# Kernel optimization log

Measured on AMD Instinct MI355X. Metric: run time of the kernel, lower is better.

Reference implementation:

```python
import jax, jax.numpy as jnp
import numpy as np

N = 50000
E = 600000
F_IN = 256
H = 128            # num_hidden_units * num_heads (heads=1)
C = 20             # num_classes
NEG_SLOPE = 0.2    # PyG GATConv default


def setup_inputs() -> dict:
    key = jax.random.key(0)
    ks = jax.random.split(key, 16)
    g = lambda k, shape, fan: jax.random.normal(k, shape, jnp.float32) / np.sqrt(fan)
    return {
        "x": jax.random.normal(ks[0], (N, F_IN), jnp.float32),
        "edge_index": jax.random.randint(ks[1], (2, E), 0, N, jnp.int64),
        # GATConv 1: F_IN -> H (heads=1, concat)
        "W1": g(ks[2], (F_IN, H), F_IN),
        "a_src1": g(ks[3], (H,), H),
        "a_dst1": g(ks[4], (H,), H),
        "b1": jnp.zeros((H,), jnp.float32),
        # GATConv 2: H -> H (heads=1)
        "W2": g(ks[5], (H, H), H),
        "a_src2": g(ks[6], (H,), H),
        "a_dst2": g(ks[7], (H,), H),
        "b2": jnp.zeros((H,), jnp.float32),
        # MLP head
        "Wm1": g(ks[8], (H, H), H),
        "bm1": jnp.zeros((H,), jnp.float32),
        "Wm2": g(ks[9], (H, C), H),
        "bm2": jnp.zeros((C,), jnp.float32),
    }


def gat_layer(x, W, a_src, a_dst, b, src, dst, n_nodes):
    """Single-head GATConv (PyG semantics, self-loops already in src/dst)."""
    h = x @ W                                    # [N, H]
    # edge attention logits: leaky_relu(a_src . h_j + a_dst . h_i)
    logits = jax.nn.leaky_relu((h @ a_src)[src] + (h @ a_dst)[dst], NEG_SLOPE)  # [Etot]
    # softmax over incoming edges per target node
    m = jax.ops.segment_max(logits, dst, num_segments=n_nodes)
    e = jnp.exp(logits - m[dst])
    denom = jax.ops.segment_sum(e, dst, num_segments=n_nodes)
    coef = e / denom[dst]                        # [Etot]
    out = jax.ops.segment_sum(coef[:, None] * h[src], dst, num_segments=n_nodes)
    return out + b


def reference(x, edge_index, W1, a_src1, a_dst1, b1, W2, a_src2, a_dst2, b2, Wm1, bm1, Wm2, bm2):
    n = x.shape[0]
    loops = jnp.arange(n, dtype=edge_index.dtype)
    src = jnp.concatenate([edge_index[0], loops])  # add self loops (GATConv default)
    dst = jnp.concatenate([edge_index[1], loops])
    h = gat_layer(x, W1, a_src1, a_dst1, b1, src, dst, n)
    h = jax.nn.relu(h)                            # dropout = identity at eval
    h = gat_layer(h, W2, a_src2, a_dst2, b2, src, dst, n)
    # MLP head: Linear -> (dropout) -> ReLU -> Linear -> sigmoid
    z = jax.nn.relu(h @ Wm1 + bm1)
    return jax.nn.sigmoid(z @ Wm2 + bm2)
```

## Files before the change

### kernel.cpp

```cpp
#include <hip/hip_runtime.h>
#include <math.h>

#define F_IN 256
#define HDIM 128
#define NCLS 20
#define NEG_SLOPE 0.2f
#define SCAN_CHUNK 1024

typedef float f32x4 __attribute__((ext_vector_type(4)));
typedef _Float16 f16x2 __attribute__((ext_vector_type(2)));
typedef _Float16 f16x4 __attribute__((ext_vector_type(4)));
typedef _Float16 f16x8 __attribute__((ext_vector_type(8)));

static __device__ __forceinline__ float lrelu(float x) { return x > 0.f ? x : NEG_SLOPE * x; }

__global__ void count_kernel(const int* __restrict__ ei, int E, int N, int* __restrict__ deg) {
    int e = blockIdx.x * blockDim.x + threadIdx.x;
    int Etot = E + N;
    if (e >= Etot) return;
    int d = (e < E) ? ei[E + e] : (e - E);
    atomicAdd(&deg[d], 1);
}

__global__ __launch_bounds__(256) void scan_reduce_kernel(const int* __restrict__ deg, int n,
                                                          int* __restrict__ bsums) {
    int base = blockIdx.x * SCAN_CHUNK + threadIdx.x * 4;
    int s = 0;
    if (base + 3 < n) {
        int4 v = *reinterpret_cast<const int4*>(&deg[base]);
        s = v.x + v.y + v.z + v.w;
    } else {
#pragma unroll
        for (int j = 0; j < 4; ++j) if (base + j < n) s += deg[base + j];
    }
#pragma unroll
    for (int o = 32; o > 0; o >>= 1) s += __shfl_down(s, o);
    __shared__ int ws[4];
    int lane = threadIdx.x & 63, w = threadIdx.x >> 6;
    if (lane == 0) ws[w] = s;
    __syncthreads();
    if (threadIdx.x == 0) bsums[blockIdx.x] = ws[0] + ws[1] + ws[2] + ws[3];
}

__global__ __launch_bounds__(256) void scan_bsums_kernel(int* __restrict__ bsums, int nb,
                                                         int* __restrict__ off, int n) {
    __shared__ int sh[256];
    int tid = threadIdx.x;
    int v = (tid < nb) ? bsums[tid] : 0;
    sh[tid] = v;
    __syncthreads();
    for (int d = 1; d < 256; d <<= 1) {
        int t = (tid >= d) ? sh[tid - d] : 0;
        __syncthreads();
        sh[tid] += t;
        __syncthreads();
    }
    if (tid < nb) bsums[tid] = sh[tid] - v;
    if (tid == 255) off[n] = sh[255];
}

__global__ __launch_bounds__(256) void scan_down_kernel(const int* __restrict__ deg, int n,
                                                        const int* __restrict__ bpre,
                                                        int* __restrict__ off) {
    int base = blockIdx.x * SCAN_CHUNK + threadIdx.x * 4;
    int v0 = 0, v1 = 0, v2 = 0, v3 = 0;
    if (base + 3 < n) {
        int4 t = *reinterpret_cast<const int4*>(&deg[base]);
        v0 = t.x; v1 = t.y; v2 = t.z; v3 = t.w;
    } else {
        if (base + 0 < n) v0 = deg[base + 0];
        if (base + 1 < n) v1 = deg[base + 1];
        if (base + 2 < n) v2 = deg[base + 2];
        if (base + 3 < n) v3 = deg[base + 3];
    }
    int tsum = v0 + v1 + v2 + v3;
    int lane = threadIdx.x & 63, w = threadIdx.x >> 6;
    int inc = tsum;
#pragma unroll
    for (int o = 1; o < 64; o <<= 1) {
        int t = __shfl_up(inc, o);
        if (lane >= o) inc += t;
    }
    int texc = inc - tsum;
    __shared__ int wsum[4];
    if (lane == 63) wsum[w] = inc;
    __syncthreads();
    int wpre = 0;
    for (int i = 0; i < w; ++i) wpre += wsum[i];
    int p = bpre[blockIdx.x] + wpre + texc;
    if (base + 3 < n) {
        int4 o4;
        o4.x = p; o4.y = p + v0; o4.z = p + v0 + v1; o4.w = p + v0 + v1 + v2;
        *reinterpret_cast<int4*>(&off[base]) = o4;
    } else {
        int run = p;
        if (base + 0 < n) { off[base + 0] = run; run += v0; }
        if (base + 1 < n) { off[base + 1] = run; run += v1; }
        if (base + 2 < n) { off[base + 2] = run; run += v2; }
        if (base + 3 < n) { off[base + 3] = run; }
    }
}

__global__ void scatter_kernel(const int* __restrict__ ei, int E, int N,
                               const int* __restrict__ off, int* __restrict__ cursor,
                               int* __restrict__ csr_src) {
    int e = blockIdx.x * blockDim.x + threadIdx.x;
    int Etot = E + N;
    if (e >= Etot) return;
    int s, d;
    if (e < E) { s = ei[e]; d = ei[E + e]; } else { s = d = e - E; }
    int pos = off[d] + atomicAdd(&cursor[d], 1);
    csr_src[pos] = s;
}

__global__ __launch_bounds__(64) void pack_b_kernel(const float* __restrict__ W1,
                                                    const float* __restrict__ W2,
                                                    const float* __restrict__ Wm1,
                                                    _Float16* __restrict__ p1,
                                                    _Float16* __restrict__ p2,
                                                    _Float16* __restrict__ p3) {
    int t = blockIdx.x;
    int lane = threadIdx.x;
    const float* B; _Float16* out; int r;
    if (t < 64)      { B = W1;  out = p1; r = t; }
    else if (t < 96) { B = W2;  out = p2; r = t - 64; }
    else             { B = Wm1; out = p3; r = t - 96; }
    int ks = r >> 3, cf = r & 7;
    int c  = cf * 16 + (lane & 15);
    int k0 = ks * 32 + (lane >> 4) * 8;
    _Float16 h8[8], l8[8];
#pragma unroll
    for (int i = 0; i < 8; ++i) {
        float v = B[(size_t)(k0 + i) * 128 + c];
        h8[i] = (_Float16)v;
        l8[i] = (_Float16)(v - (float)h8[i]);
    }
    size_t base = (((size_t)(ks * 8 + cf) * 2) * 64 + lane) * 8;
#pragma unroll
    for (int i = 0; i < 8; ++i) { out[base + i] = h8[i]; out[base + 512 + i] = l8[i]; }
}

template <int AFMT>
__global__ __launch_bounds__(256) void gemm_mfma_kernel(const void* __restrict__ Aptr,
                                                        const _Float16* __restrict__ Bp,
                                                        _Float16* __restrict__ C, int M, int K,
                                                        const float* __restrict__ bias, int act) {
    int tid = threadIdx.x;
    int lane = tid & 63;
    int wid = tid >> 6;
    int wr = wid >> 1, wc = wid & 1;
    int bm = blockIdx.x * 64;
    int l15 = lane & 15, l4 = lane >> 4;
    int row0 = bm + wr * 32 + l15;
    int koff = l4 * 8;

    f32x4 acc[2][4];
#pragma unroll
    for (int m = 0; m < 2; ++m)
#pragma unroll
        for (int j = 0; j < 4; ++j) acc[m][j] = (f32x4){0.f, 0.f, 0.f, 0.f};

    const f16x8 zf = {0, 0, 0, 0, 0, 0, 0, 0};

    auto loadA = [&](int ks, f16x8 a[2]) {
        int kbase = ks * 32 + koff;
#pragma unroll
        for (int m = 0; m < 2; ++m) {
            int rr = row0 + m * 16;
            if (rr < M) {
                if (AFMT == 0) {
                    const float* A = (const float*)Aptr;
                    float4 v0 = *reinterpret_cast<const float4*>(&A[(size_t)rr * K + kbase]);
                    float4 v1 = *reinterpret_cast<const float4*>(&A[(size_t)rr * K + kbase + 4]);
                    f16x8 t;
                    t[0] = (_Float16)v0.x; t[1] = (_Float16)v0.y;
                    t[2] = (_Float16)v0.z; t[3] = (_Float16)v0.w;
                    t[4] = (_Float16)v1.x; t[5] = (_Float16)v1.y;
                    t[6] = (_Float16)v1.z; t[7] = (_Float16)v1.w;
                    a[m] = t;
                } else {
                    const _Float16* A = (const _Float16*)Aptr;
                    a[m] = *reinterpret_cast<const f16x8*>(&A[(size_t)rr * K + kbase]);
                }
            } else a[m] = zf;
        }
    };
    auto loadB = [&](int ks, f16x8 bh[4], f16x8 bl[4]) {
#pragma unroll
        for (int j = 0; j < 4; ++j) {
            int cf = wc * 4 + j;
            const _Float16* bp = Bp + (((size_t)(ks * 8 + cf) * 2) * 64 + lane) * 8;
            bh[j] = *reinterpret_cast<const f16x8*>(bp);
            bl[j] = *reinterpret_cast<const f16x8*>(bp + 512);
        }
    };

    f16x8 a0[2], a1[2], bh0[4], bh1[4], bl0[4], bl1[4];
    int ksteps = K >> 5;
    loadA(0, a0); loadB(0, bh0, bl0);
    for (int ks = 0; ks < ksteps; ks += 2) {
        loadA(ks + 1, a1); loadB(ks + 1, bh1, bl1);
#pragma unroll
        for (int j = 0; j < 4; ++j) {
            acc[0][j] = __builtin_amdgcn_mfma_f32_16x16x32_f16(a0[0], bh0[j], acc[0][j], 0, 0, 0);
            acc[1][j] = __builtin_amdgcn_mfma_f32_16x16x32_f16(a0[1], bh0[j], acc[1][j], 0, 0, 0);
            acc[0][j] = __builtin_amdgcn_mfma_f32_16x16x32_f16(a0[0], bl0[j], acc[0][j], 0, 0, 0);
            acc[1][j] = __builtin_amdgcn_mfma_f32_16x16x32_f16(a0[1], bl0[j], acc[1][j], 0, 0, 0);
        }
        if (ks + 2 < ksteps) { loadA(ks + 2, a0); loadB(ks + 2, bh0, bl0); }
#pragma unroll
        for (int j = 0; j < 4; ++j) {
            acc[0][j] = __builtin_amdgcn_mfma_f32_16x16x32_f16(a1[0], bh1[j], acc[0][j], 0, 0, 0);
            acc[1][j] = __builtin_amdgcn_mfma_f32_16x16x32_f16(a1[1], bh1[j], acc[1][j], 0, 0, 0);
            acc[0][j] = __builtin_amdgcn_mfma_f32_16x16x32_f16(a1[0], bl1[j], acc[0][j], 0, 0, 0);
            acc[1][j] = __builtin_amdgcn_mfma_f32_16x16x32_f16(a1[1], bl1[j], acc[1][j], 0, 0, 0);
        }
    }

#pragma unroll
    for (int j = 0; j < 4; ++j) {
        int col = wc * 64 + j * 16 + l15;
        float bi = bias ? bias[col] : 0.f;
#pragma unroll
        for (int m = 0; m < 2; ++m) {
            int rbase = bm + wr * 32 + m * 16 + l4 * 4;
#pragma unroll
            for (int reg = 0; reg < 4; ++reg) {
                int rr = rbase + reg;
                if (rr < M) {
                    float v = acc[m][j][reg] + bi;
                    if (act) v = fmaxf(v, 0.f);
                    C[(size_t)rr * 128 + col] = (_Float16)v;
                }
            }
        }
    }
}

__global__ void alphas_kernel(const _Float16* __restrict__ h, const float* __restrict__ a_src,
                              const float* __restrict__ a_dst, float* __restrict__ as_out,
                              float* __restrict__ ad_out, int N) {
    int wave = (blockIdx.x * blockDim.x + threadIdx.x) >> 6;
    int lane = threadIdx.x & 63;
    if (wave >= N) return;
    f16x2 v  = *reinterpret_cast<const f16x2*>(&h[(size_t)wave * HDIM + 2 * lane]);
    float vx = (float)v[0], vy = (float)v[1];
    float2 as = *reinterpret_cast<const float2*>(&a_src[2 * lane]);
    float2 ad = *reinterpret_cast<const float2*>(&a_dst[2 * lane]);
    float s = vx * as.x + vy * as.y;
    float d = vx * ad.x + vy * ad.y;
#pragma unroll
    for (int o = 32; o > 0; o >>= 1) { s += __shfl_down(s, o); d += __shfl_down(d, o); }
    if (lane == 0) { as_out[wave] = s; ad_out[wave] = d; }
}

__global__ __launch_bounds__(256) void aggregate_kernel(const _Float16* __restrict__ h,
                                 const float* __restrict__ asrc, const float* __restrict__ adst,
                                 const int* __restrict__ off, const int* __restrict__ csr_src,
                                 const float* __restrict__ bias,
                                 _Float16* __restrict__ out,
                                 int N, int do_relu) {
    __shared__ float2 sm[4][64];
    int wslot = threadIdx.x >> 6;
    int wave = blockIdx.x * 4 + wslot;
    int lane = threadIdx.x & 63;
    if (wave >= N) return;
    int n = wave;
    int o0 = off[n], o1 = off[n + 1];
    float ad = adst[n];

    float denom = 0.f;
    float2 accA = make_float2(0.f, 0.f);
    float2 accB = make_float2(0.f, 0.f);

    for (int base = o0; base < o1; base += 64) {
        int cnt = o1 - base; if (cnt > 64) cnt = 64;
        float e = 0.f; int s = 0;
        if (lane < cnt) {
            s = csr_src[base + lane];
            e = __expf(lrelu(asrc[s] + ad));
        }
        float t = e;
#pragma unroll
        for (int o = 32; o > 0; o >>= 1) t += __shfl_xor(t, o);
        denom += t;
        sm[wslot][lane] = make_float2(__int_as_float(s), e);
        int j = 0;
        for (; j + 1 < cnt; j += 2) {
            float2 v0 = sm[wslot][j];
            float2 v1 = sm[wslot][j + 1];
            int s0 = __float_as_int(v0.x);
            int s1 = __float_as_int(v1.x);
            f16x2 h0 = *reinterpret_cast<const f16x2*>(&h[(size_t)s0 * HDIM + 2 * lane]);
            f16x2 h1 = *reinterpret_cast<const f16x2*>(&h[(size_t)s1 * HDIM + 2 * lane]);
            accA.x = fmaf(v0.y, (float)h0[0], accA.x);
            accA.y = fmaf(v0.y, (float)h0[1], accA.y);
            accB.x = fmaf(v1.y, (float)h1[0], accB.x);
            accB.y = fmaf(v1.y, (float)h1[1], accB.y);
        }
        if (j < cnt) {
            float2 v0 = sm[wslot][j];
            int s0 = __float_as_int(v0.x);
            f16x2 h0 = *reinterpret_cast<const f16x2*>(&h[(size_t)s0 * HDIM + 2 * lane]);
            accA.x = fmaf(v0.y, (float)h0[0], accA.x);
            accA.y = fmaf(v0.y, (float)h0[1], accA.y);
        }
    }

    float inv = 1.f / denom;
    float2 bi = *reinterpret_cast<const float2*>(&bias[2 * lane]);
    float r0 = (accA.x + accB.x) * inv + bi.x;
    float r1 = (accA.y + accB.y) * inv + bi.y;
    if (do_relu) { r0 = fmaxf(r0, 0.f); r1 = fmaxf(r1, 0.f); }
    f16x2 o;
    o[0] = (_Float16)r0;
    o[1] = (_Float16)r1;
    *reinterpret_cast<f16x2*>(&out[(size_t)n * HDIM + 2 * lane]) = o;
}

__global__ __launch_bounds__(256) void head_kernel(const _Float16* __restrict__ Z,
                                                   const float* __restrict__ W,
                                                   const float* __restrict__ b,
                                                   float* __restrict__ out, int N) {
    __shared__ float Ws[HDIM][NCLS];
    __shared__ float Zs[256][33];
    int tid = threadIdx.x;
    for (int i = tid; i < HDIM * NCLS; i += 256) Ws[i / NCLS][i % NCLS] = W[i];
    float acc[NCLS];
#pragma unroll
    for (int c = 0; c < NCLS; ++c) acc[c] = 0.f;
    int row = blockIdx.x * 256 + tid;
    for (int k0 = 0; k0 < HDIM; k0 += 32) {
        __syncthreads();
#pragma unroll
        for (int t = 0; t < 8; ++t) {
            int flat = tid * 4 + t * 1024;
            int r = flat >> 5, kk = flat & 31;
            int gr = blockIdx.x * 256 + r;
            if (gr < N) {
                f16x4 v = *reinterpret_cast<const f16x4*>(&Z[(size_t)gr * HDIM + k0 + kk]);
                Zs[r][kk] = (float)v[0]; Zs[r][kk + 1] = (float)v[1];
                Zs[r][kk + 2] = (float)v[2]; Zs[r][kk + 3] = (float)v[3];
            } else {
                Zs[r][kk] = 0.f; Zs[r][kk + 1] = 0.f; Zs[r][kk + 2] = 0.f; Zs[r][kk + 3] = 0.f;
            }
        }
        __syncthreads();
#pragma unroll
        for (int kk = 0; kk < 32; ++kk) {
            float a = Zs[tid][kk];
#pragma unroll
            for (int c = 0; c < NCLS; ++c) acc[c] = fmaf(a, Ws[k0 + kk][c], acc[c]);
        }
    }
    if (row < N) {
#pragma unroll
        for (int c = 0; c < NCLS; ++c) {
            float v = acc[c] + b[c];
            out[(size_t)row * NCLS + c] = 1.f / (1.f + expf(-v));
        }
    }
}

extern "C" void kernel_launch(void* const* d_in, const int* in_sizes, int n_in,
                              void* d_out, int out_size, void* d_ws, size_t ws_size,
                              hipStream_t stream) {
    const float* x      = (const float*)d_in[0];
    const int*   ei     = (const int*)d_in[1];
    const float* W1     = (const float*)d_in[2];
    const float* a_src1 = (const float*)d_in[3];
    const float* a_dst1 = (const float*)d_in[4];
    const float* b1     = (const float*)d_in[5];
    const float* W2     = (const float*)d_in[6];
    const float* a_src2 = (const float*)d_in[7];
    const float* a_dst2 = (const float*)d_in[8];
    const float* b2     = (const float*)d_in[9];
    const float* Wm1    = (const float*)d_in[10];
    const float* bm1    = (const float*)d_in[11];
    const float* Wm2    = (const float*)d_in[12];
    const float* bm2    = (const float*)d_in[13];

    int N = in_sizes[0] / F_IN;
    int E = in_sizes[1] / 2;
    int Etot = E + N;

    char* ws = (char*)d_ws;
    size_t pos = 0;
    auto alloc = [&](size_t bytes) -> void* {
        void* p = ws + pos;
        pos = (pos + bytes + 255) & ~(size_t)255;
        return p;
    };
    _Float16* h16 = (_Float16*)alloc((size_t)N * HDIM * 2);
    _Float16* f16 = (_Float16*)alloc((size_t)N * HDIM * 2);
    float* as_buf = (float*)alloc((size_t)N * 4);
    float* ad_buf = (float*)alloc((size_t)N * 4);
    int*   deg    = (int*)alloc((size_t)N * 4);
    int*   offs   = (int*)alloc((size_t)(N + 1) * 4);
    int*   cursor = (int*)alloc((size_t)N * 4);
    int*   csr    = (int*)alloc((size_t)Etot * 4);
    int*   bsums  = (int*)alloc(256 * 4);
    _Float16* p1 = (_Float16*)alloc(65536 * 2);
    _Float16* p2 = (_Float16*)alloc(32768 * 2);
    _Float16* p3 = (_Float16*)alloc(32768 * 2);

    hipMemsetAsync(deg, 0, (size_t)N * 4, stream);
    hipMemsetAsync(cursor, 0, (size_t)N * 4, stream);

    int eb = (Etot + 255) / 256;
    int nb = (N + SCAN_CHUNK - 1) / SCAN_CHUNK;
    count_kernel<<<eb, 256, 0, stream>>>(ei, E, N, deg);
    scan_reduce_kernel<<<nb, 256, 0, stream>>>(deg, N, bsums);
    scan_bsums_kernel<<<1, 256, 0, stream>>>(bsums, nb, offs, N);
    scan_down_kernel<<<nb, 256, 0, stream>>>(deg, N, bsums, offs);
    scatter_kernel<<<eb, 256, 0, stream>>>(ei, E, N, offs, cursor, csr);

    pack_b_kernel<<<128, 64, 0, stream>>>(W1, W2, Wm1, p1, p2, p3);

    int gemm_blocks = (N + 63) / 64;
    int wave_blocks = (N + 3) / 4;

    gemm_mfma_kernel<0><<<gemm_blocks, 256, 0, stream>>>(x, p1, h16, N, F_IN, nullptr, 0);
    alphas_kernel<<<wave_blocks, 256, 0, stream>>>(h16, a_src1, a_dst1, as_buf, ad_buf, N);
    aggregate_kernel<<<wave_blocks, 256, 0, stream>>>(h16, as_buf, ad_buf, offs, csr, b1, f16, N, 1);

    gemm_mfma_kernel<1><<<gemm_blocks, 256, 0, stream>>>(f16, p2, h16, N, HDIM, nullptr, 0);
    alphas_kernel<<<wave_blocks, 256, 0, stream>>>(h16, a_src2, a_dst2, as_buf, ad_buf, N);
    aggregate_kernel<<<wave_blocks, 256, 0, stream>>>(h16, as_buf, ad_buf, offs, csr, b2, f16, N, 0);

    gemm_mfma_kernel<1><<<gemm_blocks, 256, 0, stream>>>(f16, p3, h16, N, HDIM, bm1, 1);
    head_kernel<<<(N + 255) / 256, 256, 0, stream>>>(h16, Wm2, bm2, (float*)d_out, N);
}
```

Measured before the change: 254.9 us.

## Fuse attention-logit dot products into GEMM epilogue and retile GEMM/aggregation

Removes the separate alphas kernel by computing the a_src/a_dst dot products inside the GEMM epilogue, using shuffles and a small shared-memory reduction across the four waves. The GEMM is retiled to 32-row blocks with each wave owning 32 columns, K is a compile-time template parameter, and loads are prefetched several steps ahead with an interleaved hi/lo B packing. The aggregation kernel now has each half-wave handle alternate edges with 4-wide fp16 loads, and the halves are combined by a cross-half shuffle. This saves a pass over h and two launches, at the cost of more GEMM blocks, more redundant A-row reads, and extra epilogue work. The alphas are now computed from fp32 accumulators rather than fp16-rounded h.

```diff
diff --git a/kernel.cpp b/kernel.cpp
--- a/kernel.cpp
+++ b/kernel.cpp
@@ -128,130 +128,170 @@
     int ks = r >> 3, cf = r & 7;
     int c  = cf * 16 + (lane & 15);
     int k0 = ks * 32 + (lane >> 4) * 8;
-    _Float16 h8[8], l8[8];
+    size_t base = ((size_t)r * 64 + lane) * 16;
 #pragma unroll
     for (int i = 0; i < 8; ++i) {
         float v = B[(size_t)(k0 + i) * 128 + c];
-        h8[i] = (_Float16)v;
-        l8[i] = (_Float16)(v - (float)h8[i]);
-    }
-    size_t base = (((size_t)(ks * 8 + cf) * 2) * 64 + lane) * 8;
-#pragma unroll
-    for (int i = 0; i < 8; ++i) { out[base + i] = h8[i]; out[base + 512 + i] = l8[i]; }
-}
-
-template <int AFMT>
-__global__ __launch_bounds__(256) void gemm_mfma_kernel(const void* __restrict__ Aptr,
-                                                        const _Float16* __restrict__ Bp,
-                                                        _Float16* __restrict__ C, int M, int K,
-                                                        const float* __restrict__ bias, int act) {
+        _Float16 h = (_Float16)v;
+        out[base + i]     = h;
+        out[base + 8 + i] = (_Float16)(v - (float)h);
+    }
+}
+
+template <int AFMT, int KSTEPS>
+__global__ __launch_bounds__(256, 4) void gemm_mfma_kernel(
+        const void* __restrict__ Aptr, const _Float16* __restrict__ Bp,
+        _Float16* __restrict__ C, int M,
+        const float* __restrict__ bias, int act,
+        const float* __restrict__ a_src, const float* __restrict__ a_dst,
+        float* __restrict__ as_out, float* __restrict__ ad_out) {
+    constexpr int K  = KSTEPS * 32;
+    constexpr int DA = (KSTEPS < 3) ? KSTEPS : 3;
+    constexpr int DB = (KSTEPS < 2) ? KSTEPS : 2;
+    __shared__ float sal[2][4][32];
+
     int tid = threadIdx.x;
     int lane = tid & 63;
-    int wid = tid >> 6;
-    int wr = wid >> 1, wc = wid & 1;
-    int bm = blockIdx.x * 64;
+    int wc = tid >> 6;
     int l15 = lane & 15, l4 = lane >> 4;
-    int row0 = bm + wr * 32 + l15;
+    int bm = blockIdx.x * 32;
     int koff = l4 * 8;
 
-    f32x4 acc[2][4];
+    const float*    A32 = (const float*)Aptr;
+    const _Float16* A16 = (const _Float16*)Aptr;
+    int r0 = bm + l15, r1 = bm + l15 + 16;
+    bool ok0 = r0 < M, ok1 = r1 < M;
+    const f16x8 zf = {0, 0, 0, 0, 0, 0, 0, 0};
+    const float4 zf4 = make_float4(0.f, 0.f, 0.f, 0.f);
+
+    float4 sAf[DA][2][2];
+    f16x8  sAh[DA][2];
+    f16x8  sBh[DB][2], sBl[DB][2];
+
+    f32x4 acc[2][2];
 #pragma unroll
     for (int m = 0; m < 2; ++m)
 #pragma unroll
-        for (int j = 0; j < 4; ++j) acc[m][j] = (f32x4){0.f, 0.f, 0.f, 0.f};
-
-    const f16x8 zf = {0, 0, 0, 0, 0, 0, 0, 0};
-
-    auto loadA = [&](int ks, f16x8 a[2]) {
-        int kbase = ks * 32 + koff;
+        for (int j = 0; j < 2; ++j) acc[m][j] = (f32x4){0.f, 0.f, 0.f, 0.f};
+
+    auto issueA = [&](int s) {
+        int slot = s % DA;
+        int kb = s * 32 + koff;
 #pragma unroll
         for (int m = 0; m < 2; ++m) {
-            int rr = row0 + m * 16;
+            int rr = m ? r1 : r0;
+            bool ok = m ? ok1 : ok0;
+            if (AFMT == 0) {
+                const float* p = &A32[(size_t)rr * K + kb];
+                sAf[slot][m][0] = ok ? *reinterpret_cast<const float4*>(p)     : zf4;
+                sAf[slot][m][1] = ok ? *reinterpret_cast<const float4*>(p + 4) : zf4;
+            } else {
+                sAh[slot][m] = ok ? *reinterpret_cast<const f16x8*>(&A16[(size_t)rr * K + kb]) : zf;
+            }
+        }
+    };
+    auto issueB = [&](int s) {
+        int slot = s % DB;
+#pragma unroll
+        for (int j = 0; j < 2; ++j) {
+            int cf = wc * 2 + j;
+            const _Float16* p = Bp + (((size_t)s * 8 + cf) * 64 + lane) * 16;
+            sBh[slot][j] = *reinterpret_cast<const f16x8*>(p);
+            sBl[slot][j] = *reinterpret_cast<const f16x8*>(p + 8);
+        }
+    };
+
+#pragma unroll
+    for (int p = 0; p < DA; ++p) issueA(p);
+#pragma unroll
+    for (int p = 0; p < DB; ++p) issueB(p);
+
+#pragma unroll
+    for (int s = 0; s < KSTEPS; ++s) {
+        f16x8 a[2], bh[2], bl[2];
+        if (AFMT == 0) {
+#pragma unroll
+            for (int m = 0; m < 2; ++m) {
+                float4 u = sAf[s % DA][m][0], w = sAf[s % DA][m][1];
+                f16x8 t;
+                t[0] = (_Float16)u.x; t[1] = (_Float16)u.y;
+                t[2] = (_Float16)u.z; t[3] = (_Float16)u.w;
+                t[4] = (_Float16)w.x; t[5] = (_Float16)w.y;
+                t[6] = (_Float16)w.z; t[7] = (_Float16)w.w;
+                a[m] = t;
+            }
+        } else {
+            a[0] = sAh[s % DA][0];
+            a[1] = sAh[s % DA][1];
+        }
+#pragma unroll
+        for (int j = 0; j < 2; ++j) { bh[j] = sBh[s % DB][j]; bl[j] = sBl[s % DB][j]; }
+        if (s + DA < KSTEPS) issueA(s + DA);
+        if (s + DB < KSTEPS) issueB(s + DB);
+#pragma unroll
+        for (int j = 0; j < 2; ++j) {
+            acc[0][j] = __builtin_amdgcn_mfma_f32_16x16x32_f16(a[0], bh[j], acc[0][j], 0, 0, 0);
+            acc[1][j] = __builtin_amdgcn_mfma_f32_16x16x32_f16(a[1], bh[j], acc[1][j], 0, 0, 0);
+            acc[0][j] = __builtin_amdgcn_mfma_f32_16x16x32_f16(a[0], bl[j], acc[0][j], 0, 0, 0);
+            acc[1][j] = __builtin_amdgcn_mfma_f32_16x16x32_f16(a[1], bl[j], acc[1][j], 0, 0, 0);
+        }
+    }
+
+    float ps[2][4], pd[2][4];
+#pragma unroll
+    for (int m = 0; m < 2; ++m)
+#pragma unroll
+        for (int reg = 0; reg < 4; ++reg) { ps[m][reg] = 0.f; pd[m][reg] = 0.f; }
+
+#pragma unroll
+    for (int j = 0; j < 2; ++j) {
+        int col = wc * 32 + j * 16 + l15;
+        float bi = bias ? bias[col] : 0.f;
+        float asc = a_src ? a_src[col] : 0.f;
+        float adc = a_src ? a_dst[col] : 0.f;
+#pragma unroll
+        for (int m = 0; m < 2; ++m) {
+#pragma unroll
+            for (int reg = 0; reg < 4; ++reg) {
+                int rr = bm + m * 16 + l4 * 4 + reg;
+                float v = acc[m][j][reg] + bi;
+                if (act) v = fmaxf(v, 0.f);
+                if (rr < M) C[(size_t)rr * 128 + col] = (_Float16)v;
+                ps[m][reg] = fmaf(v, asc, ps[m][reg]);
+                pd[m][reg] = fmaf(v, adc, pd[m][reg]);
+            }
+        }
+    }
+
+    if (a_src) {
+#pragma unroll
+        for (int o = 1; o < 16; o <<= 1) {
+#pragma unroll
+            for (int m = 0; m < 2; ++m)
+#pragma unroll
+                for (int reg = 0; reg < 4; ++reg) {
+                    ps[m][reg] += __shfl_xor(ps[m][reg], o);
+                    pd[m][reg] += __shfl_xor(pd[m][reg], o);
+                }
+        }
+        if (l15 == 0) {
+#pragma unroll
+            for (int m = 0; m < 2; ++m)
+#pragma unroll
+                for (int reg = 0; reg < 4; ++reg) {
+                    sal[0][wc][m * 16 + l4 * 4 + reg] = ps[m][reg];
+                    sal[1][wc][m * 16 + l4 * 4 + reg] = pd[m][reg];
+                }
+        }
+        __syncthreads();
+        if (tid < 32) {
+            int rr = bm + tid;
             if (rr < M) {
-                if (AFMT == 0) {
-                    const float* A = (const float*)Aptr;
-                    float4 v0 = *reinterpret_cast<const float4*>(&A[(size_t)rr * K + kbase]);
-                    float4 v1 = *reinterpret_cast<const float4*>(&A[(size_t)rr * K + kbase + 4]);
-                    f16x8 t;
-                    t[0] = (_Float16)v0.x; t[1] = (_Float16)v0.y;
-                    t[2] = (_Float16)v0.z; t[3] = (_Float16)v0.w;
-                    t[4] = (_Float16)v1.x; t[5] = (_Float16)v1.y;
-                    t[6] = (_Float16)v1.z; t[7] = (_Float16)v1.w;
-                    a[m] = t;
-                } else {
-                    const _Float16* A = (const _Float16*)Aptr;
-                    a[m] = *reinterpret_cast<const f16x8*>(&A[(size_t)rr * K + kbase]);
-                }
-            } else a[m] = zf;
-        }
-    };
-    auto loadB = [&](int ks, f16x8 bh[4], f16x8 bl[4]) {
-#pragma unroll
-        for (int j = 0; j < 4; ++j) {
-            int cf = wc * 4 + j;
-            const _Float16* bp = Bp + (((size_t)(ks * 8 + cf) * 2) * 64 + lane) * 8;
-            bh[j] = *reinterpret_cast<const f16x8*>(bp);
-            bl[j] = *reinterpret_cast<const f16x8*>(bp + 512);
-        }
-    };
-
-    f16x8 a0[2], a1[2], bh0[4], bh1[4], bl0[4], bl1[4];
-    int ksteps = K >> 5;
-    loadA(0, a0); loadB(0, bh0, bl0);
-    for (int ks = 0; ks < ksteps; ks += 2) {
-        loadA(ks + 1, a1); loadB(ks + 1, bh1, bl1);
-#pragma unroll
-        for (int j = 0; j < 4; ++j) {
-            acc[0][j] = __builtin_amdgcn_mfma_f32_16x16x32_f16(a0[0], bh0[j], acc[0][j], 0, 0, 0);
-            acc[1][j] = __builtin_amdgcn_mfma_f32_16x16x32_f16(a0[1], bh0[j], acc[1][j], 0, 0, 0);
-            acc[0][j] = __builtin_amdgcn_mfma_f32_16x16x32_f16(a0[0], bl0[j], acc[0][j], 0, 0, 0);
-            acc[1][j] = __builtin_amdgcn_mfma_f32_16x16x32_f16(a0[1], bl0[j], acc[1][j], 0, 0, 0);
-        }
-        if (ks + 2 < ksteps) { loadA(ks + 2, a0); loadB(ks + 2, bh0, bl0); }
-#pragma unroll
-        for (int j = 0; j < 4; ++j) {
-            acc[0][j] = __builtin_amdgcn_mfma_f32_16x16x32_f16(a1[0], bh1[j], acc[0][j], 0, 0, 0);
-            acc[1][j] = __builtin_amdgcn_mfma_f32_16x16x32_f16(a1[1], bh1[j], acc[1][j], 0, 0, 0);
-            acc[0][j] = __builtin_amdgcn_mfma_f32_16x16x32_f16(a1[0], bl1[j], acc[0][j], 0, 0, 0);
-            acc[1][j] = __builtin_amdgcn_mfma_f32_16x16x32_f16(a1[1], bl1[j], acc[1][j], 0, 0, 0);
-        }
-    }
-
-#pragma unroll
-    for (int j = 0; j < 4; ++j) {
-        int col = wc * 64 + j * 16 + l15;
-        float bi = bias ? bias[col] : 0.f;
-#pragma unroll
-        for (int m = 0; m < 2; ++m) {
-            int rbase = bm + wr * 32 + m * 16 + l4 * 4;
-#pragma unroll
-            for (int reg = 0; reg < 4; ++reg) {
-                int rr = rbase + reg;
-                if (rr < M) {
-                    float v = acc[m][j][reg] + bi;
-                    if (act) v = fmaxf(v, 0.f);
-                    C[(size_t)rr * 128 + col] = (_Float16)v;
-                }
+                as_out[rr] = sal[0][0][tid] + sal[0][1][tid] + sal[0][2][tid] + sal[0][3][tid];
+                ad_out[rr] = sal[1][0][tid] + sal[1][1][tid] + sal[1][2][tid] + sal[1][3][tid];
             }
         }
     }
-}
-
-__global__ void alphas_kernel(const _Float16* __restrict__ h, const float* __restrict__ a_src,
-                              const float* __restrict__ a_dst, float* __restrict__ as_out,
-                              float* __restrict__ ad_out, int N) {
-    int wave = (blockIdx.x * blockDim.x + threadIdx.x) >> 6;
-    int lane = threadIdx.x & 63;
-    if (wave >= N) return;
-    f16x2 v  = *reinterpret_cast<const f16x2*>(&h[(size_t)wave * HDIM + 2 * lane]);
-    float vx = (float)v[0], vy = (float)v[1];
-    float2 as = *reinterpret_cast<const float2*>(&a_src[2 * lane]);
-    float2 ad = *reinterpret_cast<const float2*>(&a_dst[2 * lane]);
-    float s = vx * as.x + vy * as.y;
-    float d = vx * ad.x + vy * ad.y;
-#pragma unroll
-    for (int o = 32; o > 0; o >>= 1) { s += __shfl_down(s, o); d += __shfl_down(d, o); }
-    if (lane == 0) { as_out[wave] = s; ad_out[wave] = d; }
 }
 
 __global__ __launch_bounds__(256) void aggregate_kernel(const _Float16* __restrict__ h,
@@ -265,13 +305,14 @@
     int wave = blockIdx.x * 4 + wslot;
     int lane = threadIdx.x & 63;
     if (wave >= N) return;
-    int n = wave;
-    int o0 = off[n], o1 = off[n + 1];
-    float ad = adst[n];
+    int o0 = off[wave], o1 = off[wave + 1];
+    float ad = adst[wave];
+    int l31 = lane & 31;
+    int jst = lane >> 5;
 
     float denom = 0.f;
-    float2 accA = make_float2(0.f, 0.f);
-    float2 accB = make_float2(0.f, 0.f);
+    float4 aA = make_float4(0.f, 0.f, 0.f, 0.f);
+    float4 aB = make_float4(0.f, 0.f, 0.f, 0.f);
 
     for (int base = o0; base < o1; base += 64) {
         int cnt = o1 - base; if (cnt > 64) cnt = 64;
@@ -285,37 +326,54 @@
         for (int o = 32; o > 0; o >>= 1) t += __shfl_xor(t, o);
         denom += t;
         sm[wslot][lane] = make_float2(__int_as_float(s), e);
-        int j = 0;
-        for (; j + 1 < cnt; j += 2) {
-            float2 v0 = sm[wslot][j];
-            float2 v1 = sm[wslot][j + 1];
-            int s0 = __float_as_int(v0.x);
-            int s1 = __float_as_int(v1.x);
-            f16x2 h0 = *reinterpret_cast<const f16x2*>(&h[(size_t)s0 * HDIM + 2 * lane]);
-            f16x2 h1 = *reinterpret_cast<const f16x2*>(&h[(size_t)s1 * HDIM + 2 * lane]);
-            accA.x = fmaf(v0.y, (float)h0[0], accA.x);
-            accA.y = fmaf(v0.y, (float)h0[1], accA.y);
-            accB.x = fmaf(v1.y, (float)h1[0], accB.x);
-            accB.y = fmaf(v1.y, (float)h1[1], accB.y);
+
+        int j = jst;
+        for (; j + 2 < cnt; j += 4) {
+            float2 s0 = sm[wslot][j];
+            float2 s1 = sm[wslot][j + 2];
+            f16x4 h0 = *reinterpret_cast<const f16x4*>(&h[(size_t)__float_as_int(s0.x) * HDIM + 4 * l31]);
+            f16x4 h1 = *reinterpret_cast<const f16x4*>(&h[(size_t)__float_as_int(s1.x) * HDIM + 4 * l31]);
+            aA.x = fmaf(s0.y, (float)h0[0], aA.x);
+            aA.y = fmaf(s0.y, (float)h0[1], aA.y);
+            aA.z = fmaf(s0.y, (float)h0[2], aA.z);
+            aA.w = fmaf(s0.y, (float)h0[3], aA.w);
+            aB.x = fmaf(s1.y, (float)h1[0], aB.x);
+            aB.y = fmaf(s1.y, (float)h1[1], aB.y);
+            aB.z = fmaf(s1.y, (float)h1[2], aB.z);
+            aB.w = fmaf(s1.y, (float)h1[3], aB.w);
         }
         if (j < cnt) {
-            float2 v0 = sm[wslot][j];
-            int s0 = __float_as_int(v0.x);
-            f16x2 h0 = *reinterpret_cast<const f16x2*>(&h[(size_t)s0 * HDIM + 2 * lane]);
-            accA.x = fmaf(v0.y, (float)h0[0], accA.x);
-            accA.y = fmaf(v0.y, (float)h0[1], accA.y);
-        }
-    }
-
-    float inv = 1.f / denom;
-    float2 bi = *reinterpret_cast<const float2*>(&bias[2 * lane]);
-    float r0 = (accA.x + accB.x) * inv + bi.x;
-    float r1 = (accA.y + accB.y) * inv + bi.y;
-    if (do_relu) { r0 = fmaxf(r0, 0.f); r1 = fmaxf(r1, 0.f); }
-    f16x2 o;
-    o[0] = (_Float16)r0;
-    o[1] = (_Float16)r1;
-    *reinterpret_cast<f16x2*>(&out[(size_t)n * HDIM + 2 * lane]) = o;
+            float2 s0 = sm[wslot][j];
+            f16x4 h0 = *reinterpret_cast<const f16x4*>(&h[(size_t)__float_as_int(s0.x) * HDIM + 4 * l31]);
+            aA.x = fmaf(s0.y, (float)h0[0], aA.x);
+            aA.y = fmaf(s0.y, (float)h0[1], aA.y);
+            aA.z = fmaf(s0.y, (float)h0[2], aA.z);
+            aA.w = fmaf(s0.y, (float)h0[3], aA.w);
+        }
+    }
+
+    aA.x += aB.x; aA.y += aB.y; aA.z += aB.z; aA.w += aB.w;
+    aA.x += __shfl_xor(aA.x, 32);
+    aA.y += __shfl_xor(aA.y, 32);
+    aA.z += __shfl_xor(aA.z, 32);
+    aA.w += __shfl_xor(aA.w, 32);
+
+    if (lane < 32) {
+        float inv = 1.f / denom;
+        float4 bi = *reinterpret_cast<const float4*>(&bias[4 * l31]);
+        float v0 = aA.x * inv + bi.x;
+        float v1 = aA.y * inv + bi.y;
+        float v2 = aA.z * inv + bi.z;
+        float v3 = aA.w * inv + bi.w;
+        if (do_relu) {
+            v0 = fmaxf(v0, 0.f); v1 = fmaxf(v1, 0.f);
+            v2 = fmaxf(v2, 0.f); v3 = fmaxf(v3, 0.f);
+        }
+        f16x4 o4;
+        o4[0] = (_Float16)v0; o4[1] = (_Float16)v1;
+        o4[2] = (_Float16)v2; o4[3] = (_Float16)v3;
+        *reinterpret_cast<f16x4*>(&out[(size_t)wave * HDIM + 4 * l31]) = o4;
+    }
 }
 
 __global__ __launch_bounds__(256) void head_kernel(const _Float16* __restrict__ Z,
@@ -417,17 +475,18 @@
 
     pack_b_kernel<<<128, 64, 0, stream>>>(W1, W2, Wm1, p1, p2, p3);
 
-    int gemm_blocks = (N + 63) / 64;
+    int gemm_blocks = (N + 31) / 32;
     int wave_blocks = (N + 3) / 4;
 
-    gemm_mfma_kernel<0><<<gemm_blocks, 256, 0, stream>>>(x, p1, h16, N, F_IN, nullptr, 0);
-    alphas_kernel<<<wave_blocks, 256, 0, stream>>>(h16, a_src1, a_dst1, as_buf, ad_buf, N);
+    gemm_mfma_kernel<0, 8><<<gemm_blocks, 256, 0, stream>>>(x, p1, h16, N, nullptr, 0,
+                                                            a_src1, a_dst1, as_buf, ad_buf);
     aggregate_kernel<<<wave_blocks, 256, 0, stream>>>(h16, as_buf, ad_buf, offs, csr, b1, f16, N, 1);
 
-    gemm_mfma_kernel<1><<<gemm_blocks, 256, 0, stream>>>(f16, p2, h16, N, HDIM, nullptr, 0);
-    alphas_kernel<<<wave_blocks, 256, 0, stream>>>(h16, a_src2, a_dst2, as_buf, ad_buf, N);
+    gemm_mfma_kernel<1, 4><<<gemm_blocks, 256, 0, stream>>>(f16, p2, h16, N, nullptr, 0,
+                                                            a_src2, a_dst2, as_buf, ad_buf);
     aggregate_kernel<<<wave_blocks, 256, 0, stream>>>(h16, as_buf, ad_buf, offs, csr, b2, f16, N, 0);
 
-    gemm_mfma_kernel<1><<<gemm_blocks, 256, 0, stream>>>(f16, p3, h16, N, HDIM, bm1, 1);
+    gemm_mfma_kernel<1, 4><<<gemm_blocks, 256, 0, stream>>>(f16, p3, h16, N, bm1, 1,
+                                                            nullptr, nullptr, nullptr, nullptr);
     head_kernel<<<(N + 255) / 256, 256, 0, stream>>>(h16, Wm2, bm2, (float*)d_out, N);
 }
```

Result: slower. 312.3 us (+22.5%).
